# Kernel tuning notes

Measured on AMD Instinct MI355X. Metric: run time of the kernel, lower is better.

The kernel has to match this reference:

```python
import jax, jax.numpy as jnp
import numpy as np

WAVEFORM_TICKS = 512
BIN_SIGMA = 5.0
NX, NY = 48, 48
GAUSS_NORM = 0.3989422804  # 1/sqrt(2*pi)
EL_NORM = 2.5066           # sqrt(2*pi) as hard-coded in the module
B, NE = 4, 5000
H1, H2 = 64, 128


def setup_inputs() -> dict:
    key = jax.random.key(0)
    ks = jax.random.split(key, 8)
    simulator_input = 0.5 * jax.random.normal(ks[0], (B, NE, 2), dtype=jnp.float32)
    z_positions = jax.random.uniform(ks[1], (B, NE), dtype=jnp.float32) * (WAVEFORM_TICKS - 1)
    mask = jax.random.uniform(ks[2], (B, NE), dtype=jnp.float32)
    # MLP params: 2 -> 64 -> 128 -> 1
    W1 = jax.random.normal(ks[3], (2, H1), dtype=jnp.float32) * (1.0 / np.sqrt(2.0))
    b1 = jnp.zeros((H1,), jnp.float32)
    W2 = jax.random.normal(ks[4], (H1, H2), dtype=jnp.float32) * (1.0 / np.sqrt(H1))
    b2 = jnp.zeros((H2,), jnp.float32)
    W3 = jax.random.normal(ks[5], (H2, 1), dtype=jnp.float32) * (1.0 / np.sqrt(H2))
    b3 = jnp.zeros((1,), jnp.float32)
    # learned EL spread scalar, init 0.1 as in the module
    el_spread = 0.1 * jnp.ones((1,), jnp.float32)
    # SiPM grid locations in [-1, 1]^2 -> (NX, NY, 2)
    ax = jnp.linspace(-1.0, 1.0, NX, dtype=jnp.float32)
    ay = jnp.linspace(-1.0, 1.0, NY, dtype=jnp.float32)
    gx, gy = jnp.meshgrid(ax, ay, indexing='ij')
    sensor_locations = jnp.stack([gx, gy], axis=-1)
    return {"simulator_input": simulator_input, "z_positions": z_positions, "mask": mask,
            "W1": W1, "b1": b1, "W2": W2, "b2": b2, "W3": W3, "b3": b3,
            "el_spread": el_spread, "sensor_locations": sensor_locations}


def reference(simulator_input, z_positions, mask, W1, b1, W2, b2, W3, b3, el_spread, sensor_locations):
    # MLP per-electron light yield: (B, NE, 2) -> (B, NE)
    h = jax.nn.relu(simulator_input @ W1 + b1)
    h = jax.nn.relu(h @ W2 + b2)
    response = (h @ W3 + b3)[..., 0]

    # spatial gaussian spread onto the sensor grid: (B, NE, NX, NY)
    diff = simulator_input[:, :, None, None, :] - sensor_locations  # (B,NE,NX,NY,2)
    r_squared = jnp.sum(diff * diff, axis=-1)
    es = el_spread[0]
    sipm_spread = 100.0 * jnp.exp(-0.5 * r_squared / (es * es)) / (es * EL_NORM)
    sensor_response = sipm_spread * response[:, :, None, None]  # (B,NE,NX,NY)

    # time-domain gaussian binning: (B, NE, T)
    t = jnp.arange(WAVEFORM_TICKS, dtype=simulator_input.dtype)
    ev = jnp.exp(-((t[None, None, :] - z_positions[..., None]) ** 2) / (2.0 * BIN_SIGMA))
    ev = ev * (GAUSS_NORM / np.sqrt(BIN_SIGMA))
    ev = ev * mask[..., None]

    # contract over electrons: (B,T,NE) x (B,NE,NX*NY) -> (B,T,NX*NY)
    sens_flat = sensor_response.reshape(B, NE, NX * NY)
    wf = jnp.einsum('bet,bes->bts', ev, sens_flat)
    wf = wf.reshape(B, WAVEFORM_TICKS, NX, NY).transpose(0, 2, 3, 1)  # (B,NX,NY,T)
    return wf.sum(axis=0)  # (NX, NY, T)
```

## Files before the change

kernel.cpp:

```cpp
#include <hip/hip_runtime.h>
#include <math.h>

#define NXg 48
#define NYg 48
#define Tg 512
#define NG 20000
#define H1g 64
#define H2g 128

#define TT 32
#define NBINS 16
#define RCAP 3072
#define CCAP (RCAP / 32)
#define SPLIT 3
#define KSPLIT 8
#define NSB 36
#define E2 2
#define EB 256

#define KSCALE 0.84932180028802f

typedef float vf16 __attribute__((ext_vector_type(16)));
typedef _Float16 half8 __attribute__((ext_vector_type(8)));
typedef float floatx4 __attribute__((ext_vector_type(4)));

#define OFF_BFRAG  0
#define OFF_POSC   (OFF_BFRAG  + (size_t)NBINS*CCAP*4*512*2)
#define OFF_PART   (OFF_POSC   + (size_t)NBINS*RCAP*8)
#define OFF_RESP8  (OFF_PART   + (size_t)SPLIT*NSB*NBINS*2048*4)
#define OFF_EDATA  (OFF_RESP8  + (size_t)NG*8*4)
#define OFF_EDATA2 (OFF_EDATA  + (size_t)NG*16)
#define OFF_LIST   (OFF_EDATA2 + (size_t)NG*16)
#define OFF_CNT    (OFF_LIST   + (size_t)NBINS*RCAP*4)

__global__ __launch_bounds__(EB) void k_mlp(
    const float* __restrict__ sim, const float* __restrict__ zpos,
    const float* __restrict__ mask,
    const float* __restrict__ W1, const float* __restrict__ b1,
    const float* __restrict__ W2, const float* __restrict__ b2,
    const float* __restrict__ W3, const float* __restrict__ b3,
    float4* __restrict__ edata, float* __restrict__ resp8,
    int* __restrict__ cnt)
{
    __shared__ __align__(64) float sW2[H1g][16];
    __shared__ float4 sW1b[H1g];

    int tid = threadIdx.x;
    int q = blockIdx.y;
    int k0 = q * 16;

    if (blockIdx.x == 0 && q == 0 && tid < NBINS) cnt[tid] = 0;

    if (tid < H1g)
        sW1b[tid] = make_float4(W1[tid], W1[H1g + tid], b1[tid], 0.0f);
    if (tid < 256) {
        int j = tid >> 2, c = (tid & 3) * 4;
        *(float4*)&sW2[j][c] = *(const float4*)&W2[j * H2g + k0 + c];
    }
    __syncthreads();

    int g0 = blockIdx.x * EB + tid;
    if (g0 >= NG / E2) return;
    int g1 = g0 + NG / E2;

    float2 s0 = *(const float2*)&sim[2 * g0];
    float2 s1 = *(const float2*)&sim[2 * g1];

    vf16 a0 = *(const vf16*)&b2[k0];
    vf16 a1 = a0;
#pragma unroll 4
    for (int j = 0; j < H1g; ++j) {
        float4 wb = sW1b[j];
        float h0 = fmaxf(fmaf(s0.x, wb.x, fmaf(s0.y, wb.y, wb.z)), 0.0f);
        float h1 = fmaxf(fmaf(s1.x, wb.x, fmaf(s1.y, wb.y, wb.z)), 0.0f);
        vf16 w = *(const vf16*)sW2[j];
#pragma unroll
        for (int u = 0; u < 16; ++u) {
            a0[u] = fmaf(h0, w[u], a0[u]);
            a1[u] = fmaf(h1, w[u], a1[u]);
        }
    }

    float r0 = (q == 0) ? b3[0] : 0.0f;
    float r1 = r0;
#pragma unroll
    for (int u = 0; u < 16; ++u) {
        float w3 = W3[k0 + u];
        r0 = fmaf(fmaxf(a0[u], 0.0f), w3, r0);
        r1 = fmaf(fmaxf(a1[u], 0.0f), w3, r1);
    }
    resp8[(size_t)q * NG + g0] = r0;
    resp8[(size_t)q * NG + g1] = r1;

    if (q == 0) {
        edata[g0] = make_float4(s0.x, s0.y, zpos[g0], mask[g0]);
        edata[g1] = make_float4(s1.x, s1.y, zpos[g1], mask[g1]);
    }
}

__global__ __launch_bounds__(256) void k_bins(
    const float4* __restrict__ edata, const float* __restrict__ resp8,
    const float* __restrict__ el_spread,
    int* __restrict__ cnt, int* __restrict__ list, float4* __restrict__ edata2)
{
    __shared__ int lcnt[NBINS], lbase[NBINS];
    int tid = threadIdx.x;
    if (tid < NBINS) lcnt[tid] = 0;
    __syncthreads();

    int g = blockIdx.x * 256 + tid;
    int jlo = 0, jhi = -1;
    int off[3];
    if (g < NG) {
        float4 E = edata[g];
        float s = 0.0f;
#pragma unroll
        for (int q = 0; q < KSPLIT; ++q) s += resp8[(size_t)q * NG + g];
        float es = el_spread[0];
        float amp = s * E.w * (100.0f / (es * 2.5066f)) *
                    (0.3989422804f / 2.23606797749979f);
        float kk = KSCALE / es;
        edata2[g] = make_float4(E.x * kk, E.y * kk, E.z, amp);

        float z = E.z;
        jlo = max((int)ceilf((z - 44.5f) * (1.0f / 32.0f)), 0);
        jhi = min((int)floorf((z + 13.5f) * (1.0f / 32.0f)), NBINS - 1);
        for (int j = jlo; j <= jhi; ++j)
            off[j - jlo] = atomicAdd(&lcnt[j], 1);
    }
    __syncthreads();
    if (tid < NBINS) {
        int c = lcnt[tid];
        lbase[tid] = c ? atomicAdd(&cnt[tid], c) : 0;
    }
    __syncthreads();
    for (int j = jlo; j <= jhi; ++j) {
        int p = lbase[j] + off[j - jlo];
        if (p < RCAP) list[j * RCAP + p] = g;
    }
}

__global__ __launch_bounds__(256) void k_prof(
    const float4* __restrict__ edata2, const int* __restrict__ cnt,
    const int* __restrict__ list,
    _Float16* __restrict__ bfrag, float2* __restrict__ posc)
{
    __shared__ float4 sE[64];
    int bin = blockIdx.y;
    int tid = threadIdx.x;
    int count = min(cnt[bin], RCAP);
    int nch = (count + 31) >> 5;
    int cbase = blockIdx.x * 2;
    if (cbase >= nch) return;

    if (tid < 64) {
        int i = cbase * 32 + tid;
        float4 E = make_float4(1.0e3f, 1.0e3f, 0.0f, 0.0f);
        if (i < count) E = edata2[list[bin * RCAP + i]];
        sE[tid] = E;
        if (i < nch * 32)
            posc[(size_t)bin * RCAP + i] = make_float2(E.x, E.y);
    }
    __syncthreads();

    int ch = cbase + (tid >> 7);
    if (ch >= nch) return;
    int nt = (tid >> 6) & 1;
    int lane = tid & 63;
    int quad = lane >> 4, t16 = lane & 15;
    float tt = (float)(bin * TT + nt * 16 + t16);

    half8 hi, lo;
#pragma unroll
    for (int j = 0; j < 8; ++j) {
        float4 E = sE[(tid >> 7) * 32 + quad * 8 + j];
        float d = tt - E.z;
        float v = E.w * __expf(-0.1f * d * d);
        _Float16 h = (_Float16)v;
        hi[j] = h;
        lo[j] = (_Float16)(v - (float)h);
    }
    size_t base = ((size_t)(bin * CCAP + ch)) * 4 * 512;
    *(half8*)&bfrag[base + (size_t)nt * 512 + lane * 8] = hi;
    *(half8*)&bfrag[base + (size_t)(2 + nt) * 512 + lane * 8] = lo;
}

__global__ __launch_bounds__(256) void k_main(
    const _Float16* __restrict__ bfrag, const float2* __restrict__ posc,
    const int* __restrict__ cnt, const float* __restrict__ el_spread,
    const float* __restrict__ sensors, float* __restrict__ part)
{
    int tid = threadIdx.x;
    int wv = tid >> 6, lane = tid & 63;
    int sb = blockIdx.x, bin = blockIdx.y, split = blockIdx.z;
    int quad = lane >> 4;

    int sA = sb * 64 + wv * 16 + (lane & 15);
    float es = el_spread[0];
    float kk = KSCALE / es;
    float sxA = sensors[2 * sA] * kk, syA = sensors[2 * sA + 1] * kk;

    int count = min(cnt[bin], RCAP);
    int nch = (count + 31) >> 5;
    int c0 = nch * split / SPLIT, c1 = nch * (split + 1) / SPLIT;

    floatx4 d0 = {0.f, 0.f, 0.f, 0.f}, d1 = {0.f, 0.f, 0.f, 0.f};

    const half8* bbase = (const half8*)bfrag + (size_t)bin * CCAP * 256 + lane;
    const float4* pbase = (const float4*)(posc + (size_t)bin * RCAP) + quad * 4;

#define LOADC(c, F0, F1, F2, F3, Q0, Q1, Q2, Q3)                          \
    {                                                                     \
        const half8* bb = bbase + (size_t)(c) * 256;                      \
        F0 = bb[0]; F1 = bb[64]; F2 = bb[128]; F3 = bb[192];              \
        const float4* pp = pbase + (size_t)(c) * 16;                      \
        Q0 = pp[0]; Q1 = pp[1]; Q2 = pp[2]; Q3 = pp[3];                   \
    }

#define COMP(F0, F1, F2, F3, Q0, Q1, Q2, Q3)                              \
    {                                                                     \
        float exs[8] = {Q0.x, Q0.z, Q1.x, Q1.z, Q2.x, Q2.z, Q3.x, Q3.z};  \
        float eys[8] = {Q0.y, Q0.w, Q1.y, Q1.w, Q2.y, Q2.w, Q3.y, Q3.w};  \
        half8 ah, al;                                                     \
        _Pragma("unroll")                                                 \
        for (int j = 0; j < 8; ++j) {                                     \
            float dx = sxA - exs[j], dy = syA - eys[j];                   \
            float d2 = fmaf(dy, dy, dx * dx);                             \
            float e = __builtin_amdgcn_exp2f(-d2);                        \
            _Float16 h = (_Float16)e;                                     \
            ah[j] = h;                                                    \
            al[j] = (_Float16)(e - (float)h);                             \
        }                                                                 \
        d0 = __builtin_amdgcn_mfma_f32_16x16x32_f16(ah, F0, d0, 0, 0, 0); \
        d1 = __builtin_amdgcn_mfma_f32_16x16x32_f16(ah, F1, d1, 0, 0, 0); \
        d0 = __builtin_amdgcn_mfma_f32_16x16x32_f16(al, F0, d0, 0, 0, 0); \
        d1 = __builtin_amdgcn_mfma_f32_16x16x32_f16(al, F1, d1, 0, 0, 0); \
        d0 = __builtin_amdgcn_mfma_f32_16x16x32_f16(ah, F2, d0, 0, 0, 0); \
        d1 = __builtin_amdgcn_mfma_f32_16x16x32_f16(ah, F3, d1, 0, 0, 0); \
    }

    if (c0 < c1) {
        half8 fA0, fA1, fA2, fA3, fB0, fB1, fB2, fB3;
        float4 qA0, qA1, qA2, qA3, qB0, qB1, qB2, qB3;
        LOADC(c0, fA0, fA1, fA2, fA3, qA0, qA1, qA2, qA3);
        int c = c0;
        for (; c + 1 < c1; c += 2) {
            LOADC(c + 1, fB0, fB1, fB2, fB3, qB0, qB1, qB2, qB3);
            COMP(fA0, fA1, fA2, fA3, qA0, qA1, qA2, qA3);
            int cn = (c + 2 < c1) ? c + 2 : c1 - 1;
            LOADC(cn, fA0, fA1, fA2, fA3, qA0, qA1, qA2, qA3);
            COMP(fB0, fB1, fB2, fB3, qB0, qB1, qB2, qB3);
        }
        if (c < c1) COMP(fA0, fA1, fA2, fA3, qA0, qA1, qA2, qA3);
    }
#undef LOADC
#undef COMP

    float* pb = part + (((size_t)split * NSB + sb) * NBINS + bin) * 2048;
    int n0 = lane & 15;
#pragma unroll
    for (int r = 0; r < 4; ++r) {
        int sl = wv * 16 + quad * 4 + r;
        pb[sl * 32 + n0]      = d0[r];
        pb[sl * 32 + 16 + n0] = d1[r];
    }
}

__global__ __launch_bounds__(256) void k_reduce(
    const float4* __restrict__ part, float* __restrict__ out)
{
    int sb = blockIdx.x, bin = blockIdx.y, tid = threadIdx.x;
#pragma unroll
    for (int h = 0; h < 2; ++h) {
        int p = h * 256 + tid;
        int sl = p >> 3, q = p & 7;
        float4 s = make_float4(0.f, 0.f, 0.f, 0.f);
        for (int sp = 0; sp < SPLIT; ++sp) {
            float4 v = part[(((size_t)sp * NSB + sb) * NBINS + bin) * 512 + p];
            s.x += v.x; s.y += v.y; s.z += v.z; s.w += v.w;
        }
        int sensor = sb * 64 + sl;
        *(float4*)(out + (size_t)sensor * Tg + bin * TT + q * 4) = s;
    }
}

extern "C" void kernel_launch(void* const* d_in, const int* in_sizes, int n_in,
                              void* d_out, int out_size, void* d_ws, size_t ws_size,
                              hipStream_t stream)
{
    const float* sim       = (const float*)d_in[0];
    const float* zpos      = (const float*)d_in[1];
    const float* mask      = (const float*)d_in[2];
    const float* W1        = (const float*)d_in[3];
    const float* b1        = (const float*)d_in[4];
    const float* W2        = (const float*)d_in[5];
    const float* b2        = (const float*)d_in[6];
    const float* W3        = (const float*)d_in[7];
    const float* b3        = (const float*)d_in[8];
    const float* el_spread = (const float*)d_in[9];
    const float* sensors   = (const float*)d_in[10];
    float* out = (float*)d_out;

    char* ws = (char*)d_ws;
    _Float16* bfrag  = (_Float16*)(ws + OFF_BFRAG);
    float2*   posc   = (float2*)(ws + OFF_POSC);
    float*    part   = (float*)(ws + OFF_PART);
    float*    resp8  = (float*)(ws + OFF_RESP8);
    float4*   edata  = (float4*)(ws + OFF_EDATA);
    float4*   edata2 = (float4*)(ws + OFF_EDATA2);
    int*      list   = (int*)(ws + OFF_LIST);
    int*      cnt    = (int*)(ws + OFF_CNT);

    k_mlp<<<dim3((NG / E2 + EB - 1) / EB, KSPLIT), EB, 0, stream>>>(
        sim, zpos, mask, W1, b1, W2, b2, W3, b3, edata, resp8, cnt);

    k_bins<<<(NG + 255) / 256, 256, 0, stream>>>(
        edata, resp8, el_spread, cnt, list, edata2);

    k_prof<<<dim3(CCAP / 2, NBINS), 256, 0, stream>>>(
        edata2, cnt, list, bfrag, posc);

    k_main<<<dim3(NSB, NBINS, SPLIT), 256, 0, stream>>>(
        bfrag, posc, cnt, el_spread, sensors, part);

    k_reduce<<<dim3(NSB, NBINS), 256, 0, stream>>>((const float4*)part, out);
}
```

Before: 140.9 us.

## Double sensor tile per wave to reuse B fragments and stage positions in LDS

Each wave now computes two 16-sensor tiles (128 sensors per block, NSB halved), so every loaded time-gaussian B fragment feeds twice as many MFMAs. Electron positions for the block's chunk range are copied once into shared memory instead of being re-read from global per chunk. The partial buffer and the reduce kernel are resized to match. The trade-off is higher register pressure from four accumulators and half as many blocks, which could reduce occupancy and parallelism.

```diff
diff --git a/kernel.cpp b/kernel.cpp
--- a/kernel.cpp
+++ b/kernel.cpp
@@ -14,7 +14,7 @@
 #define CCAP (RCAP / 32)
 #define SPLIT 3
 #define KSPLIT 8
-#define NSB 36
+#define NSB 18
 #define E2 2
 #define EB 256
 
@@ -27,7 +27,7 @@
 #define OFF_BFRAG  0
 #define OFF_POSC   (OFF_BFRAG  + (size_t)NBINS*CCAP*4*512*2)
 #define OFF_PART   (OFF_POSC   + (size_t)NBINS*RCAP*8)
-#define OFF_RESP8  (OFF_PART   + (size_t)SPLIT*NSB*NBINS*2048*4)
+#define OFF_RESP8  (OFF_PART   + (size_t)SPLIT*NSB*NBINS*4096*4)
 #define OFF_EDATA  (OFF_RESP8  + (size_t)NG*8*4)
 #define OFF_EDATA2 (OFF_EDATA  + (size_t)NG*16)
 #define OFF_LIST   (OFF_EDATA2 + (size_t)NG*16)
@@ -190,53 +190,71 @@
     const int* __restrict__ cnt, const float* __restrict__ el_spread,
     const float* __restrict__ sensors, float* __restrict__ part)
 {
+    __shared__ float4 sPos[512];
+
     int tid = threadIdx.x;
     int wv = tid >> 6, lane = tid & 63;
     int sb = blockIdx.x, bin = blockIdx.y, split = blockIdx.z;
     int quad = lane >> 4;
 
-    int sA = sb * 64 + wv * 16 + (lane & 15);
-    float es = el_spread[0];
-    float kk = KSCALE / es;
-    float sxA = sensors[2 * sA] * kk, syA = sensors[2 * sA + 1] * kk;
-
     int count = min(cnt[bin], RCAP);
     int nch = (count + 31) >> 5;
     int c0 = nch * split / SPLIT, c1 = nch * (split + 1) / SPLIT;
-
-    floatx4 d0 = {0.f, 0.f, 0.f, 0.f}, d1 = {0.f, 0.f, 0.f, 0.f};
+    int nc = c1 - c0;
+
+    {
+        const float4* psrc = (const float4*)(posc + (size_t)bin * RCAP + c0 * 32);
+        for (int i = tid; i < nc * 16; i += 256) sPos[i] = psrc[i];
+    }
+    __syncthreads();
+
+    int sA = sb * 128 + wv * 32 + (lane & 15);
+    float es = el_spread[0];
+    float kk = KSCALE / es;
+    float sx0 = sensors[2 * sA] * kk,        sy0 = sensors[2 * sA + 1] * kk;
+    float sx1 = sensors[2 * (sA + 16)] * kk, sy1 = sensors[2 * (sA + 16) + 1] * kk;
+
+    floatx4 d00 = {0.f,0.f,0.f,0.f}, d01 = {0.f,0.f,0.f,0.f};
+    floatx4 d10 = {0.f,0.f,0.f,0.f}, d11 = {0.f,0.f,0.f,0.f};
 
     const half8* bbase = (const half8*)bfrag + (size_t)bin * CCAP * 256 + lane;
-    const float4* pbase = (const float4*)(posc + (size_t)bin * RCAP) + quad * 4;
+    const float4* lbase = sPos + quad * 4;
 
 #define LOADC(c, F0, F1, F2, F3, Q0, Q1, Q2, Q3)                          \
     {                                                                     \
         const half8* bb = bbase + (size_t)(c) * 256;                      \
         F0 = bb[0]; F1 = bb[64]; F2 = bb[128]; F3 = bb[192];              \
-        const float4* pp = pbase + (size_t)(c) * 16;                      \
-        Q0 = pp[0]; Q1 = pp[1]; Q2 = pp[2]; Q3 = pp[3];                   \
+        const float4* lp = lbase + ((c) - c0) * 16;                      \
+        Q0 = lp[0]; Q1 = lp[1]; Q2 = lp[2]; Q3 = lp[3];                   \
     }
 
 #define COMP(F0, F1, F2, F3, Q0, Q1, Q2, Q3)                              \
     {                                                                     \
         float exs[8] = {Q0.x, Q0.z, Q1.x, Q1.z, Q2.x, Q2.z, Q3.x, Q3.z};  \
         float eys[8] = {Q0.y, Q0.w, Q1.y, Q1.w, Q2.y, Q2.w, Q3.y, Q3.w};  \
-        half8 ah, al;                                                     \
+        half8 ah0, al0, ah1, al1;                                         \
         _Pragma("unroll")                                                 \
         for (int j = 0; j < 8; ++j) {                                     \
-            float dx = sxA - exs[j], dy = syA - eys[j];                   \
-            float d2 = fmaf(dy, dy, dx * dx);                             \
-            float e = __builtin_amdgcn_exp2f(-d2);                        \
-            _Float16 h = (_Float16)e;                                     \
-            ah[j] = h;                                                    \
-            al[j] = (_Float16)(e - (float)h);                             \
+            float dx0 = sx0 - exs[j], dy0 = sy0 - eys[j];                 \
+            float dx1 = sx1 - exs[j], dy1 = sy1 - eys[j];                 \
+            float e0 = __builtin_amdgcn_exp2f(-fmaf(dy0, dy0, dx0 * dx0));\
+            float e1 = __builtin_amdgcn_exp2f(-fmaf(dy1, dy1, dx1 * dx1));\
+            _Float16 h0 = (_Float16)e0, h1 = (_Float16)e1;                \
+            ah0[j] = h0; al0[j] = (_Float16)(e0 - (float)h0);             \
+            ah1[j] = h1; al1[j] = (_Float16)(e1 - (float)h1);             \
         }                                                                 \
-        d0 = __builtin_amdgcn_mfma_f32_16x16x32_f16(ah, F0, d0, 0, 0, 0); \
-        d1 = __builtin_amdgcn_mfma_f32_16x16x32_f16(ah, F1, d1, 0, 0, 0); \
-        d0 = __builtin_amdgcn_mfma_f32_16x16x32_f16(al, F0, d0, 0, 0, 0); \
-        d1 = __builtin_amdgcn_mfma_f32_16x16x32_f16(al, F1, d1, 0, 0, 0); \
-        d0 = __builtin_amdgcn_mfma_f32_16x16x32_f16(ah, F2, d0, 0, 0, 0); \
-        d1 = __builtin_amdgcn_mfma_f32_16x16x32_f16(ah, F3, d1, 0, 0, 0); \
+        d00 = __builtin_amdgcn_mfma_f32_16x16x32_f16(ah0, F0, d00, 0,0,0);\
+        d01 = __builtin_amdgcn_mfma_f32_16x16x32_f16(ah0, F1, d01, 0,0,0);\
+        d10 = __builtin_amdgcn_mfma_f32_16x16x32_f16(ah1, F0, d10, 0,0,0);\
+        d11 = __builtin_amdgcn_mfma_f32_16x16x32_f16(ah1, F1, d11, 0,0,0);\
+        d00 = __builtin_amdgcn_mfma_f32_16x16x32_f16(al0, F0, d00, 0,0,0);\
+        d01 = __builtin_amdgcn_mfma_f32_16x16x32_f16(al0, F1, d01, 0,0,0);\
+        d10 = __builtin_amdgcn_mfma_f32_16x16x32_f16(al1, F0, d10, 0,0,0);\
+        d11 = __builtin_amdgcn_mfma_f32_16x16x32_f16(al1, F1, d11, 0,0,0);\
+        d00 = __builtin_amdgcn_mfma_f32_16x16x32_f16(ah0, F2, d00, 0,0,0);\
+        d01 = __builtin_amdgcn_mfma_f32_16x16x32_f16(ah0, F3, d01, 0,0,0);\
+        d10 = __builtin_amdgcn_mfma_f32_16x16x32_f16(ah1, F2, d10, 0,0,0);\
+        d11 = __builtin_amdgcn_mfma_f32_16x16x32_f16(ah1, F3, d11, 0,0,0);\
     }
 
     if (c0 < c1) {
@@ -256,13 +274,16 @@
 #undef LOADC
 #undef COMP
 
-    float* pb = part + (((size_t)split * NSB + sb) * NBINS + bin) * 2048;
+    float* pb = part + (((size_t)split * NSB + sb) * NBINS + bin) * 4096;
     int n0 = lane & 15;
 #pragma unroll
     for (int r = 0; r < 4; ++r) {
-        int sl = wv * 16 + quad * 4 + r;
-        pb[sl * 32 + n0]      = d0[r];
-        pb[sl * 32 + 16 + n0] = d1[r];
+        int sl0 = wv * 32 + quad * 4 + r;
+        int sl1 = sl0 + 16;
+        pb[sl0 * 32 + n0]      = d00[r];
+        pb[sl0 * 32 + 16 + n0] = d01[r];
+        pb[sl1 * 32 + n0]      = d10[r];
+        pb[sl1 * 32 + 16 + n0] = d11[r];
     }
 }
 
@@ -271,15 +292,15 @@
 {
     int sb = blockIdx.x, bin = blockIdx.y, tid = threadIdx.x;
 #pragma unroll
-    for (int h = 0; h < 2; ++h) {
+    for (int h = 0; h < 4; ++h) {
         int p = h * 256 + tid;
         int sl = p >> 3, q = p & 7;
         float4 s = make_float4(0.f, 0.f, 0.f, 0.f);
         for (int sp = 0; sp < SPLIT; ++sp) {
-            float4 v = part[(((size_t)sp * NSB + sb) * NBINS + bin) * 512 + p];
+            float4 v = part[(((size_t)sp * NSB + sb) * NBINS + bin) * 1024 + p];
             s.x += v.x; s.y += v.y; s.z += v.z; s.w += v.w;
         }
-        int sensor = sb * 64 + sl;
+        int sensor = sb * 128 + sl;
         *(float4*)(out + (size_t)sensor * Tg + bin * TT + q * 4) = s;
     }
 }
```

Measured after the change: 132.0 us. 6.3% less time.
